# Kernel tuning notes

Hardware: AMD Instinct MI355X
Metric: run time of the kernel (lower is better)

The kernel has to match this reference:

```python
import jax, jax.numpy as jnp
import numpy as np
import math

B, S, D, H = 4, 1024, 1024, 16
HD = D // H  # head_size = 64
NEG = -1e9


def setup_inputs() -> dict:
    rng = jax.random.key(0)
    ks = jax.random.split(rng, 12)
    f = lambda k, shape: jax.random.normal(k, shape, dtype=jnp.float32)
    inp = {
        "query": f(ks[0], (B, S, D)),
        "key": f(ks[1], (B, S, D)),
        "value": f(ks[2], (B, S, D)),
        # rel: correlation matrix between interactions, non-negative
        "rel": jax.random.uniform(ks[3], (B, S, S), dtype=jnp.float32),
        "l1": jnp.float32(0.5),
        "l2": jnp.float32(0.5),
        # timestamp: |t_i - t_j| time gaps
        "timestamp": jax.random.uniform(ks[4], (B, S, S), dtype=jnp.float32) * 10.0,
        "encode_pos": 0,
        "pos_key_embeds": f(ks[5], (32, HD)) * 0.02,
        "pos_value_embeds": f(ks[6], (32, HD)) * 0.02,
        # causal mask: True = disallowed (future) position
        "mask": jnp.broadcast_to(jnp.triu(jnp.ones((S, S), dtype=bool), k=1), (B, S, S)),
        "Wq": f(ks[7], (D, D)) / math.sqrt(D), "bq": jnp.zeros((D,), jnp.float32),
        "Wk": f(ks[8], (D, D)) / math.sqrt(D), "bk": jnp.zeros((D,), jnp.float32),
        "Wv": f(ks[9], (D, D)) / math.sqrt(D), "bv": jnp.zeros((D,), jnp.float32),
    }
    return inp


def _split_heads(x, W, b):
    # nn.Linear uses x @ W.T + b ; reshape to [B,H,S,HD]
    y = x @ W.T + b
    return y.reshape(B, S, H, HD).transpose(0, 2, 1, 3)


def reference(query, key, value, rel, l1, l2, timestamp, encode_pos,
              pos_key_embeds, pos_value_embeds, mask,
              Wq, bq, Wk, bk, Wv, bv):
    assert encode_pos == 0, "reference implements the encode_pos=False path"
    q = _split_heads(query, Wq, bq)   # [B,H,S,HD]
    k = _split_heads(key, Wk, bk)
    v = _split_heads(value, Wv, bv)

    m = mask[:, None]  # [B,1,S,S], True = masked

    # relation-based attention: future-mask rel, softmax over nonzero entries
    relm = rel[:, None] * (~m).astype(jnp.float32)          # [B,1,S,S]
    rel_attn = jax.nn.softmax(jnp.where(relm == 0, -1e5, relm), axis=-1)

    # scaled dot-product scores
    scores = jnp.einsum("bhqd,bhkd->bhqk", q, k) / jnp.sqrt(jnp.float32(HD))
    scores = jnp.where(m, NEG, scores)
    prob_attn = jax.nn.softmax(scores, axis=-1)             # [B,H,S,S]

    # time-decay attention: exp(-|dt|), future-masked
    ts = jnp.exp(-jnp.abs(timestamp))[:, None]              # [B,1,S,S]
    ts = jnp.where(m, NEG, ts)
    time_attn = jax.nn.softmax(ts, axis=-1)

    prob = (1.0 - l2) * prob_attn + l2 * time_attn
    prob = (1.0 - l1) * prob + l1 * rel_attn                # [B,H,S,S]

    out = jnp.einsum("bhqk,bhkd->bhqd", prob, v)
    out = out.transpose(0, 2, 1, 3).reshape(B, S, D)
    return out, prob
```

## Files before the change

kernel.cpp:

```cpp
#include <hip/hip_runtime.h>
#include <cstdint>
#include <cstddef>


typedef __bf16 bf16_t;
typedef __bf16 bf16x8 __attribute__((ext_vector_type(8)));
typedef __bf16 bf16x4 __attribute__((ext_vector_type(4)));
typedef float  f32x4  __attribute__((ext_vector_type(4)));

__device__ __forceinline__ f32x4 mfma16(bf16x8 a, bf16x8 b, f32x4 c) {
  return __builtin_amdgcn_mfma_f32_16x16x32_bf16(a, b, c, 0, 0, 0);
}

__device__ __forceinline__ void g2l16(const void* g, void* l) {
  __builtin_amdgcn_global_load_lds((__attribute__((address_space(1))) void*)(g),
                                   (__attribute__((address_space(3))) void*)(l),
                                   16, 0, 0);
}

__global__ __launch_bounds__(256) void cast_kernel(
    const float* __restrict__ q, const float* __restrict__ k, const float* __restrict__ v,
    const float* __restrict__ wq, const float* __restrict__ wk, const float* __restrict__ wv,
    bf16_t* __restrict__ Xb, bf16_t* __restrict__ Wb) {
  int i = blockIdx.x * 256 + threadIdx.x;
  const float* src;
  bf16_t* dst;
  if (i < 3145728) {
    int m = i >> 20;
    size_t o = (size_t)(i & 1048575) * 4;
    src = (m == 0) ? q : (m == 1) ? k : v;
    dst = Xb + (size_t)m * 4194304 + o;
    src += o;
  } else {
    int j = i - 3145728;
    int m = j >> 18;
    size_t o = (size_t)(j & 262143) * 4;
    src = (m == 0) ? wq : (m == 1) ? wk : wv;
    dst = Wb + (size_t)m * 1048576 + o;
    src += o;
  }
  f32x4 f = *(const f32x4*)src;
  bf16x4 r;
  r[0] = (bf16_t)f[0]; r[1] = (bf16_t)f[1]; r[2] = (bf16_t)f[2]; r[3] = (bf16_t)f[3];
  *(bf16x4*)dst = r;
}

__global__ __launch_bounds__(256) void gemm_qkv(
    const bf16_t* __restrict__ Xb, const bf16_t* __restrict__ Wb,
    const float* __restrict__ bqp, const float* __restrict__ bkp, const float* __restrict__ bvp,
    bf16_t* __restrict__ Yb) {
  __shared__ __align__(16) bf16_t As[128 * 32];
  __shared__ __align__(16) bf16_t Bs[128 * 32];
  const int z = blockIdx.z;
  const bf16_t* X = Xb + (size_t)z * 4194304;
  const bf16_t* W = Wb + (size_t)z * 1048576;
  const float* bias = (z == 0) ? bqp : (z == 1) ? bkp : bvp;
  bf16_t* Y = Yb + (size_t)z * 4194304;

  const int tid = threadIdx.x;
  const int lane = tid & 63;
  const int w = tid >> 6;
  const int wr = w >> 1, wc = w & 1;
  const int rb = blockIdx.y * 128, cb = blockIdx.x * 128;
  const int lr = lane & 15, g = lane >> 4;

  f32x4 zero = {0.f, 0.f, 0.f, 0.f};
  f32x4 acc[4][4];
  for (int m = 0; m < 4; ++m)
    for (int n = 0; n < 4; ++n) acc[m][n] = zero;

  for (int k0 = 0; k0 < 1024; k0 += 32) {
    for (int r = 0; r < 2; ++r) {
      int cid = r * 256 + tid;
      int row = cid >> 2;
      int ko = (cid & 3) * 8;
      const bf16_t* ga = X + ((size_t)(rb + row) * 1024 + k0 + ko);
      const bf16_t* gb = W + ((size_t)(cb + row) * 1024 + k0 + ko);
      char* la = (char*)As + r * 4096 + w * 1024;
      char* lb = (char*)Bs + r * 4096 + w * 1024;
      g2l16(ga, la);
      g2l16(gb, lb);
    }
    asm volatile("s_waitcnt vmcnt(0)" ::: "memory");
    __syncthreads();

    bf16x8 afr[4], bfr[4];
    for (int m = 0; m < 4; ++m)
      afr[m] = *(const bf16x8*)&As[(wr * 64 + m * 16 + lr) * 32 + g * 8];
    for (int n = 0; n < 4; ++n)
      bfr[n] = *(const bf16x8*)&Bs[(wc * 64 + n * 16 + lr) * 32 + g * 8];
    for (int m = 0; m < 4; ++m)
      for (int n = 0; n < 4; ++n)
        acc[m][n] = mfma16(afr[m], bfr[n], acc[m][n]);
    __syncthreads();
  }

  for (int m = 0; m < 4; ++m) {
    int rowb = rb + wr * 64 + m * 16 + g * 4;
    for (int n = 0; n < 4; ++n) {
      int col = cb + wc * 64 + n * 16 + lr;
      float bb = bias[col];
      for (int r = 0; r < 4; ++r)
        Y[(size_t)(rowb + r) * 1024 + col] = (bf16_t)(acc[m][n][r] + bb);
    }
  }
}

__global__ __launch_bounds__(256) void transpose_v(const bf16_t* __restrict__ Yv,
                                                   bf16_t* __restrict__ vT) {
  __shared__ __align__(16) bf16_t t[64][68];
  const int bh = blockIdx.y, b = bh >> 4, h = bh & 15;
  const int s0 = blockIdx.x * 64;
  const int tid = threadIdx.x;
  for (int i = 0; i < 4; ++i) {
    int c = tid + i * 256;
    int r = c >> 4, c4 = (c & 15) * 4;
    bf16x4 v4 = *(const bf16x4*)(Yv + ((size_t)(b * 1024 + s0 + r)) * 1024 + h * 64 + c4);
    *(bf16x4*)&t[r][c4] = v4;
  }
  __syncthreads();
  for (int i = 0; i < 4; ++i) {
    int c = tid + i * 256;
    int hd = c >> 4, s4 = (c & 15) * 4;
    bf16x4 o;
    o[0] = t[s4 + 0][hd]; o[1] = t[s4 + 1][hd];
    o[2] = t[s4 + 2][hd]; o[3] = t[s4 + 3][hd];
    *(bf16x4*)(vT + ((size_t)(bh * 64 + hd)) * 1024 + s0 + s4) = o;
  }
}

__global__ __launch_bounds__(256) void base_kernel(
    const float* __restrict__ rel, const float* __restrict__ ts,
    const float* __restrict__ l1p, const float* __restrict__ l2p,
    bf16_t* __restrict__ baseb) {
  const int row = blockIdx.x;
  const int q = row & 1023;
  const int tid = threadIdx.x;
  const int w = tid >> 6;
  const float l1 = *l1p, l2 = *l2p;
  const float cr = l1, ct = (1.f - l1) * l2;

  f32x4 rv = *(const f32x4*)(rel + (size_t)row * 1024 + tid * 4);
  f32x4 tv = *(const f32x4*)(ts  + (size_t)row * 1024 + tid * 4);

  float x[4], t[4];
  for (int j = 0; j < 4; ++j) {
    int k = tid * 4 + j;
    bool msk = k > q;
    float rj = rv[j];
    x[j] = (msk || rj == 0.f) ? -100000.f : rj;
    t[j] = msk ? -1e9f : __expf(-fabsf(tv[j]));
  }
  float mr = fmaxf(fmaxf(x[0], x[1]), fmaxf(x[2], x[3]));
  float mt = fmaxf(fmaxf(t[0], t[1]), fmaxf(t[2], t[3]));
  for (int o = 1; o < 64; o <<= 1) {
    mr = fmaxf(mr, __shfl_xor(mr, o));
    mt = fmaxf(mt, __shfl_xor(mt, o));
  }
  __shared__ float red[4][4];
  if ((tid & 63) == 0) { red[0][w] = mr; red[1][w] = mt; }
  __syncthreads();
  mr = fmaxf(fmaxf(red[0][0], red[0][1]), fmaxf(red[0][2], red[0][3]));
  mt = fmaxf(fmaxf(red[1][0], red[1][1]), fmaxf(red[1][2], red[1][3]));

  float er[4], et[4], sr = 0.f, st = 0.f;
  for (int j = 0; j < 4; ++j) {
    er[j] = __expf(x[j] - mr);
    et[j] = __expf(t[j] - mt);
    sr += er[j]; st += et[j];
  }
  for (int o = 1; o < 64; o <<= 1) {
    sr += __shfl_xor(sr, o);
    st += __shfl_xor(st, o);
  }
  if ((tid & 63) == 0) { red[2][w] = sr; red[3][w] = st; }
  __syncthreads();
  sr = red[2][0] + red[2][1] + red[2][2] + red[2][3];
  st = red[3][0] + red[3][1] + red[3][2] + red[3][3];

  float isr = cr / sr, ist = ct / st;
  bf16x4 o4;
  for (int j = 0; j < 4; ++j) o4[j] = (bf16_t)(er[j] * isr + et[j] * ist);
  *(bf16x4*)(baseb + (size_t)row * 1024 + tid * 4) = o4;
}

__global__ __launch_bounds__(512) void attn_kernel(
    const bf16_t* __restrict__ qY, const bf16_t* __restrict__ kY,
    const bf16_t* __restrict__ vT, const bf16_t* __restrict__ baseb,
    const float* __restrict__ l1p, const float* __restrict__ l2p,
    float* __restrict__ outp, float* __restrict__ probp) {
  const int bid = blockIdx.x;
  const int j = bid >> 3;
  const int bh = (bid & 7) * 8 + (j & 7);
  const int qg = 31 - (j >> 3);
  const int b = bh >> 4, h = bh & 15;
  const int q0 = qg * 32;
  const int tid = threadIdx.x, lane = tid & 63, w = tid >> 6;
  const int t = w >> 2;
  const int cw = w & 3;
  const int lr = lane & 15, g = lane >> 4;
  const int qr = q0 + t * 16 + lr;
  const float l1 = *l1p, l2 = *l2p;
  const float c1 = (1.f - l1) * (1.f - l2);

  __shared__ __align__(16) union ShMem {
    bf16_t plds[8][16][36];
    float  pvred[8][16][64];
  } sh;
  __shared__ float zred[8][16];

  const bf16_t* qbase = qY + ((size_t)(b * 1024 + qr)) * 1024 + h * 64 + g * 8;
  bf16x8 bq0 = *(const bf16x8*)qbase;
  bf16x8 bq1 = *(const bf16x8*)(qbase + 32);

  const bf16_t* kptr = kY + ((size_t)(b * 1024 + lr)) * 1024 + h * 64 + g * 8;

  const int nch = (q0 + t * 16) / 32 + 1;
  f32x4 zero = {0.f, 0.f, 0.f, 0.f};

  bf16x4 esave[8][2];
  float zp = 0.f;
#pragma unroll
  for (int c = 0; c < 8; ++c) {
    const int ch = cw + 4 * c;
    if (ch < nch) {
      const bf16_t* p0 = kptr + (size_t)ch * 32768;
      bf16x8 k0 = *(const bf16x8*)p0;
      bf16x8 k1 = *(const bf16x8*)(p0 + 32);
      bf16x8 k2 = *(const bf16x8*)(p0 + 16384);
      bf16x8 k3 = *(const bf16x8*)(p0 + 16416);
      f32x4 s0 = zero, s1 = zero;
      s0 = mfma16(k0, bq0, s0);
      s0 = mfma16(k1, bq1, s0);
      s1 = mfma16(k2, bq0, s1);
      s1 = mfma16(k3, bq1, s1);
      const int kc0 = ch * 32 + g * 4;
      bf16x4 e0, e1;
      for (int r = 0; r < 4; ++r) {
        float ea = (kc0 + r > qr) ? 0.f : __expf(s0[r] * 0.125f);
        float eb = (kc0 + 16 + r > qr) ? 0.f : __expf(s1[r] * 0.125f);
        zp += ea + eb;
        e0[r] = (bf16_t)ea;
        e1[r] = (bf16_t)eb;
      }
      esave[c][0] = e0;
      esave[c][1] = e1;
    }
  }
  zp += __shfl_xor(zp, 16);
  zp += __shfl_xor(zp, 32);
  if (lane < 16) zred[w][lr] = zp;
  __syncthreads();
  const float Z = zred[t * 4 + 0][lr] + zred[t * 4 + 1][lr] +
                  zred[t * 4 + 2][lr] + zred[t * 4 + 3][lr];
  const float invz = c1 / Z;

  const bf16_t* baserow = baseb + ((size_t)(b * 1024 + qr)) * 1024;
  const bf16_t* vbase = vT + ((size_t)(bh * 64 + lr)) * 1024 + g * 8;
  float* probbase = probp + ((size_t)(bh * 1024 + q0 + t * 16)) * 1024;
  const int srow = lane >> 3, scol = (lane & 7) * 4;

  f32x4 acc[4];
  for (int cf = 0; cf < 4; ++cf) acc[cf] = zero;

#pragma unroll
  for (int c = 0; c < 8; ++c) {
    const int ch = cw + 4 * c;
    if (ch < nch) {
      bf16x8 vv[4];
      for (int cf = 0; cf < 4; ++cf)
        vv[cf] = *(const bf16x8*)(vbase + (size_t)cf * 16384 + ch * 32);
      for (int f = 0; f < 2; ++f) {
        const int kc0 = ch * 32 + f * 16 + g * 4;
        bf16x4 b4 = *(const bf16x4*)(baserow + kc0);
        bf16x4 eb = esave[c][f];
        bf16x4 pb;
        for (int r = 0; r < 4; ++r)
          pb[r] = (bf16_t)((float)eb[r] * invz + (float)b4[r]);
        *(bf16x4*)&sh.plds[w][lr][f * 16 + g * 4] = pb;
      }
      asm volatile("s_waitcnt lgkmcnt(0)" ::: "memory");
      bf16x8 pa = *(const bf16x8*)&sh.plds[w][lr][g * 8];
      bf16x4 r0 = *(const bf16x4*)&sh.plds[w][srow][scol];
      bf16x4 r1 = *(const bf16x4*)&sh.plds[w][srow + 8][scol];
      f32x4 o0, o1;
      for (int jj = 0; jj < 4; ++jj) { o0[jj] = (float)r0[jj]; o1[jj] = (float)r1[jj]; }
      float* pr = probbase + (size_t)srow * 1024 + ch * 32 + scol;
      __builtin_nontemporal_store(o0, (f32x4*)pr);
      __builtin_nontemporal_store(o1, (f32x4*)(pr + 8 * 1024));
      for (int cf = 0; cf < 4; ++cf)
        acc[cf] = mfma16(pa, vv[cf], acc[cf]);
    }
  }

  const int kstart = nch * 32;
  for (int i = 0; i < 4; ++i) {
    int qrr = q0 + t * 16 + cw * 4 + i;
    const bf16_t* brow = baseb + ((size_t)(b * 1024 + qrr)) * 1024;
    float* prow = probp + ((size_t)(bh * 1024 + qrr)) * 1024;
    for (int k = kstart + lane * 4; k < 1024; k += 256) {
      bf16x4 b4 = *(const bf16x4*)(brow + k);
      f32x4 f4;
      f4[0] = (float)b4[0]; f4[1] = (float)b4[1];
      f4[2] = (float)b4[2]; f4[3] = (float)b4[3];
      __builtin_nontemporal_store(f4, (f32x4*)(prow + k));
    }
  }

  __syncthreads();
  for (int cf = 0; cf < 4; ++cf)
    for (int r = 0; r < 4; ++r)
      sh.pvred[w][g * 4 + r][cf * 16 + lr] = acc[cf][r];
  __syncthreads();
  {
    const int gw = tid >> 6, hd = tid & 63;
    const int tt = gw >> 2;
    for (int i = 0; i < 4; ++i) {
      int rr = (gw & 3) * 4 + i;
      float s = sh.pvred[tt * 4 + 0][rr][hd] + sh.pvred[tt * 4 + 1][rr][hd] +
                sh.pvred[tt * 4 + 2][rr][hd] + sh.pvred[tt * 4 + 3][rr][hd];
      outp[((size_t)(b * 1024 + q0 + tt * 16 + rr)) * 1024 + h * 64 + hd] = s;
    }
  }
}

extern "C" void kernel_launch(void* const* d_in, const int* in_sizes, int n_in,
                              void* d_out, int out_size, void* d_ws, size_t ws_size,
                              hipStream_t stream) {
  const float* query = (const float*)d_in[0];
  const float* key   = (const float*)d_in[1];
  const float* value = (const float*)d_in[2];
  const float* rel   = (const float*)d_in[3];
  const float* l1p   = (const float*)d_in[4];
  const float* l2p   = (const float*)d_in[5];
  const float* tsp   = (const float*)d_in[6];
  const float* Wq = (const float*)d_in[11];
  const float* bq = (const float*)d_in[12];
  const float* Wk = (const float*)d_in[13];
  const float* bk = (const float*)d_in[14];
  const float* Wv = (const float*)d_in[15];
  const float* bv = (const float*)d_in[16];

  char* ws = (char*)d_ws;
  bf16_t* Xb    = (bf16_t*)(ws);
  bf16_t* Wb    = (bf16_t*)(ws + 25165824);
  bf16_t* Yb    = (bf16_t*)(ws + 31457280);
  bf16_t* vT    = (bf16_t*)(ws + 56623104);
  bf16_t* baseb = (bf16_t*)(ws + 65011712);

  float* outp  = (float*)d_out;
  float* probp = outp + 4194304;

  cast_kernel<<<dim3(15360), dim3(256), 0, stream>>>(query, key, value, Wq, Wk, Wv, Xb, Wb);
  gemm_qkv<<<dim3(8, 32, 3), dim3(256), 0, stream>>>(Xb, Wb, bq, bk, bv, Yb);
  transpose_v<<<dim3(16, 64), dim3(256), 0, stream>>>(Yb + (size_t)2 * 4194304, vT);
  base_kernel<<<dim3(4096), dim3(256), 0, stream>>>(rel, tsp, l1p, l2p, baseb);
  attn_kernel<<<dim3(2048), dim3(512), 0, stream>>>(Yb, Yb + 4194304, vT, baseb,
                                                    l1p, l2p, outp, probp);
}
```

Before: 171.9 us.

## Fuse fp32-to-bf16 cast into QKV GEMM and hoist attention loads out of branches

Removes the separate cast kernel: the QKV GEMM now reads fp32 inputs and weights directly, converts them in registers and stores bf16 into LDS, replacing the async global-to-LDS path. This saves one kernel launch and a full bf16 write and re-read of the activations and weights, at the cost of the GEMM loading twice the bytes per tile with synchronous register staging. In the attention kernel, the K, V and base loads are hoisted ahead of the causal branch using clamped chunk indices so they can be issued early. It also adds a launch-bounds occupancy hint, splits the Z accumulation across four lanes, and drops an explicit LDS waitcnt.

```diff
diff --git a/kernel.cpp b/kernel.cpp
--- a/kernel.cpp
+++ b/kernel.cpp
@@ -12,48 +12,16 @@
   return __builtin_amdgcn_mfma_f32_16x16x32_bf16(a, b, c, 0, 0, 0);
 }
 
-__device__ __forceinline__ void g2l16(const void* g, void* l) {
-  __builtin_amdgcn_global_load_lds((__attribute__((address_space(1))) void*)(g),
-                                   (__attribute__((address_space(3))) void*)(l),
-                                   16, 0, 0);
-}
-
-__global__ __launch_bounds__(256) void cast_kernel(
-    const float* __restrict__ q, const float* __restrict__ k, const float* __restrict__ v,
-    const float* __restrict__ wq, const float* __restrict__ wk, const float* __restrict__ wv,
-    bf16_t* __restrict__ Xb, bf16_t* __restrict__ Wb) {
-  int i = blockIdx.x * 256 + threadIdx.x;
-  const float* src;
-  bf16_t* dst;
-  if (i < 3145728) {
-    int m = i >> 20;
-    size_t o = (size_t)(i & 1048575) * 4;
-    src = (m == 0) ? q : (m == 1) ? k : v;
-    dst = Xb + (size_t)m * 4194304 + o;
-    src += o;
-  } else {
-    int j = i - 3145728;
-    int m = j >> 18;
-    size_t o = (size_t)(j & 262143) * 4;
-    src = (m == 0) ? wq : (m == 1) ? wk : wv;
-    dst = Wb + (size_t)m * 1048576 + o;
-    src += o;
-  }
-  f32x4 f = *(const f32x4*)src;
-  bf16x4 r;
-  r[0] = (bf16_t)f[0]; r[1] = (bf16_t)f[1]; r[2] = (bf16_t)f[2]; r[3] = (bf16_t)f[3];
-  *(bf16x4*)dst = r;
-}
-
 __global__ __launch_bounds__(256) void gemm_qkv(
-    const bf16_t* __restrict__ Xb, const bf16_t* __restrict__ Wb,
+    const float* __restrict__ qf, const float* __restrict__ kf, const float* __restrict__ vf,
+    const float* __restrict__ wqf, const float* __restrict__ wkf, const float* __restrict__ wvf,
     const float* __restrict__ bqp, const float* __restrict__ bkp, const float* __restrict__ bvp,
     bf16_t* __restrict__ Yb) {
   __shared__ __align__(16) bf16_t As[128 * 32];
   __shared__ __align__(16) bf16_t Bs[128 * 32];
   const int z = blockIdx.z;
-  const bf16_t* X = Xb + (size_t)z * 4194304;
-  const bf16_t* W = Wb + (size_t)z * 1048576;
+  const float* X = (z == 0) ? qf : (z == 1) ? kf : vf;
+  const float* W = (z == 0) ? wqf : (z == 1) ? wkf : wvf;
   const float* bias = (z == 0) ? bqp : (z == 1) ? bkp : bvp;
   bf16_t* Y = Yb + (size_t)z * 4194304;
 
@@ -74,14 +42,20 @@
       int cid = r * 256 + tid;
       int row = cid >> 2;
       int ko = (cid & 3) * 8;
-      const bf16_t* ga = X + ((size_t)(rb + row) * 1024 + k0 + ko);
-      const bf16_t* gb = W + ((size_t)(cb + row) * 1024 + k0 + ko);
-      char* la = (char*)As + r * 4096 + w * 1024;
-      char* lb = (char*)Bs + r * 4096 + w * 1024;
-      g2l16(ga, la);
-      g2l16(gb, lb);
-    }
-    asm volatile("s_waitcnt vmcnt(0)" ::: "memory");
+      const float* ga = X + ((size_t)(rb + row) * 1024 + k0 + ko);
+      const float* gb = W + ((size_t)(cb + row) * 1024 + k0 + ko);
+      f32x4 a0 = *(const f32x4*)ga;
+      f32x4 a1 = *(const f32x4*)(ga + 4);
+      f32x4 b0 = *(const f32x4*)gb;
+      f32x4 b1 = *(const f32x4*)(gb + 4);
+      bf16x8 av, bv8;
+      for (int j = 0; j < 4; ++j) {
+        av[j] = (bf16_t)a0[j]; av[4 + j] = (bf16_t)a1[j];
+        bv8[j] = (bf16_t)b0[j]; bv8[4 + j] = (bf16_t)b1[j];
+      }
+      *(bf16x8*)&As[row * 32 + ko] = av;
+      *(bf16x8*)&Bs[row * 32 + ko] = bv8;
+    }
     __syncthreads();
 
     bf16x8 afr[4], bfr[4];
@@ -184,7 +158,7 @@
   *(bf16x4*)(baseb + (size_t)row * 1024 + tid * 4) = o4;
 }
 
-__global__ __launch_bounds__(512) void attn_kernel(
+__global__ __launch_bounds__(512, 8) void attn_kernel(
     const bf16_t* __restrict__ qY, const bf16_t* __restrict__ kY,
     const bf16_t* __restrict__ vT, const bf16_t* __restrict__ baseb,
     const float* __restrict__ l1p, const float* __restrict__ l2p,
@@ -219,16 +193,17 @@
   f32x4 zero = {0.f, 0.f, 0.f, 0.f};
 
   bf16x4 esave[8][2];
-  float zp = 0.f;
+  f32x4 zacc = zero;
 #pragma unroll
   for (int c = 0; c < 8; ++c) {
     const int ch = cw + 4 * c;
+    const int cl = (ch < nch) ? ch : nch - 1;
+    const bf16_t* p0 = kptr + (size_t)cl * 32768;
+    bf16x8 k0 = *(const bf16x8*)p0;
+    bf16x8 k1 = *(const bf16x8*)(p0 + 32);
+    bf16x8 k2 = *(const bf16x8*)(p0 + 16384);
+    bf16x8 k3 = *(const bf16x8*)(p0 + 16416);
     if (ch < nch) {
-      const bf16_t* p0 = kptr + (size_t)ch * 32768;
-      bf16x8 k0 = *(const bf16x8*)p0;
-      bf16x8 k1 = *(const bf16x8*)(p0 + 32);
-      bf16x8 k2 = *(const bf16x8*)(p0 + 16384);
-      bf16x8 k3 = *(const bf16x8*)(p0 + 16416);
       f32x4 s0 = zero, s1 = zero;
       s0 = mfma16(k0, bq0, s0);
       s0 = mfma16(k1, bq1, s0);
@@ -239,7 +214,8 @@
       for (int r = 0; r < 4; ++r) {
         float ea = (kc0 + r > qr) ? 0.f : __expf(s0[r] * 0.125f);
         float eb = (kc0 + 16 + r > qr) ? 0.f : __expf(s1[r] * 0.125f);
-        zp += ea + eb;
+        zacc[r] += ea;
+        zacc[r] += eb;
         e0[r] = (bf16_t)ea;
         e1[r] = (bf16_t)eb;
       }
@@ -247,6 +223,7 @@
       esave[c][1] = e1;
     }
   }
+  float zp = (zacc[0] + zacc[1]) + (zacc[2] + zacc[3]);
   zp += __shfl_xor(zp, 16);
   zp += __shfl_xor(zp, 32);
   if (lane < 16) zred[w][lr] = zp;
@@ -266,20 +243,20 @@
 #pragma unroll
   for (int c = 0; c < 8; ++c) {
     const int ch = cw + 4 * c;
+    const int cl = (ch < nch) ? ch : nch - 1;
+    bf16x8 vv[4];
+    for (int cf = 0; cf < 4; ++cf)
+      vv[cf] = *(const bf16x8*)(vbase + (size_t)cf * 16384 + cl * 32);
+    bf16x4 b40 = *(const bf16x4*)(baserow + cl * 32 + g * 4);
+    bf16x4 b41 = *(const bf16x4*)(baserow + cl * 32 + 16 + g * 4);
     if (ch < nch) {
-      bf16x8 vv[4];
-      for (int cf = 0; cf < 4; ++cf)
-        vv[cf] = *(const bf16x8*)(vbase + (size_t)cf * 16384 + ch * 32);
-      for (int f = 0; f < 2; ++f) {
-        const int kc0 = ch * 32 + f * 16 + g * 4;
-        bf16x4 b4 = *(const bf16x4*)(baserow + kc0);
-        bf16x4 eb = esave[c][f];
-        bf16x4 pb;
-        for (int r = 0; r < 4; ++r)
-          pb[r] = (bf16_t)((float)eb[r] * invz + (float)b4[r]);
-        *(bf16x4*)&sh.plds[w][lr][f * 16 + g * 4] = pb;
+      bf16x4 pb0, pb1;
+      for (int r = 0; r < 4; ++r) {
+        pb0[r] = (bf16_t)((float)esave[c][0][r] * invz + (float)b40[r]);
+        pb1[r] = (bf16_t)((float)esave[c][1][r] * invz + (float)b41[r]);
       }
-      asm volatile("s_waitcnt lgkmcnt(0)" ::: "memory");
+      *(bf16x4*)&sh.plds[w][lr][g * 4] = pb0;
+      *(bf16x4*)&sh.plds[w][lr][16 + g * 4] = pb1;
       bf16x8 pa = *(const bf16x8*)&sh.plds[w][lr][g * 8];
       bf16x4 r0 = *(const bf16x4*)&sh.plds[w][srow][scol];
       bf16x4 r1 = *(const bf16x4*)&sh.plds[w][srow + 8][scol];
@@ -342,17 +319,15 @@
   const float* bv = (const float*)d_in[16];
 
   char* ws = (char*)d_ws;
-  bf16_t* Xb    = (bf16_t*)(ws);
-  bf16_t* Wb    = (bf16_t*)(ws + 25165824);
-  bf16_t* Yb    = (bf16_t*)(ws + 31457280);
-  bf16_t* vT    = (bf16_t*)(ws + 56623104);
-  bf16_t* baseb = (bf16_t*)(ws + 65011712);
+  bf16_t* Yb    = (bf16_t*)(ws);
+  bf16_t* vT    = (bf16_t*)(ws + 25165824);
+  bf16_t* baseb = (bf16_t*)(ws + 33554432);
 
   float* outp  = (float*)d_out;
   float* probp = outp + 4194304;
 
-  cast_kernel<<<dim3(15360), dim3(256), 0, stream>>>(query, key, value, Wq, Wk, Wv, Xb, Wb);
-  gemm_qkv<<<dim3(8, 32, 3), dim3(256), 0, stream>>>(Xb, Wb, bq, bk, bv, Yb);
+  gemm_qkv<<<dim3(8, 32, 3), dim3(256), 0, stream>>>(query, key, value, Wq, Wk, Wv,
+                                                     bq, bk, bv, Yb);
   transpose_v<<<dim3(16, 64), dim3(256), 0, stream>>>(Yb + (size_t)2 * 4194304, vT);
   base_kernel<<<dim3(4096), dim3(256), 0, stream>>>(rel, tsp, l1p, l2p, baseb);
   attn_kernel<<<dim3(2048), dim3(512), 0, stream>>>(Yb, Yb + 4194304, vT, baseb,
```

Result: slower. 193.9 us (+12.8%).

## Fuse V transpose into QKV GEMM epilogue and double GEMM K-step

Applied to the files above, without the earlier changes.

The separate transpose_v kernel is removed. The QKV GEMM epilogue for the V projection now writes each 4-row accumulator fragment straight into the head-major transposed vT layout, which saves a kernel launch and a round trip of V through global memory. The GEMM main loop also loads a 64-wide K slab per barrier pair instead of 32, which halves the number of synchronisations but doubles the shared memory per block and may lower occupancy.

```diff
diff --git a/kernel.cpp b/kernel.cpp
--- a/kernel.cpp
+++ b/kernel.cpp
@@ -48,9 +48,9 @@
 __global__ __launch_bounds__(256) void gemm_qkv(
     const bf16_t* __restrict__ Xb, const bf16_t* __restrict__ Wb,
     const float* __restrict__ bqp, const float* __restrict__ bkp, const float* __restrict__ bvp,
-    bf16_t* __restrict__ Yb) {
-  __shared__ __align__(16) bf16_t As[128 * 32];
-  __shared__ __align__(16) bf16_t Bs[128 * 32];
+    bf16_t* __restrict__ Yb, bf16_t* __restrict__ vT) {
+  __shared__ __align__(16) bf16_t As[2 * 128 * 32];
+  __shared__ __align__(16) bf16_t Bs[2 * 128 * 32];
   const int z = blockIdx.z;
   const bf16_t* X = Xb + (size_t)z * 4194304;
   const bf16_t* W = Wb + (size_t)z * 1048576;
@@ -69,63 +69,58 @@
   for (int m = 0; m < 4; ++m)
     for (int n = 0; n < 4; ++n) acc[m][n] = zero;
 
-  for (int k0 = 0; k0 < 1024; k0 += 32) {
-    for (int r = 0; r < 2; ++r) {
-      int cid = r * 256 + tid;
-      int row = cid >> 2;
-      int ko = (cid & 3) * 8;
+  for (int k0 = 0; k0 < 1024; k0 += 64) {
+    for (int r = 0; r < 4; ++r) {
+      const int hh = r >> 1;
+      const int cid = (r & 1) * 256 + tid;
+      const int row = cid >> 2;
+      const int ko = (cid & 3) * 8 + hh * 32;
       const bf16_t* ga = X + ((size_t)(rb + row) * 1024 + k0 + ko);
       const bf16_t* gb = W + ((size_t)(cb + row) * 1024 + k0 + ko);
-      char* la = (char*)As + r * 4096 + w * 1024;
-      char* lb = (char*)Bs + r * 4096 + w * 1024;
+      char* la = (char*)As + hh * 8192 + (r & 1) * 4096 + w * 1024;
+      char* lb = (char*)Bs + hh * 8192 + (r & 1) * 4096 + w * 1024;
       g2l16(ga, la);
       g2l16(gb, lb);
     }
     asm volatile("s_waitcnt vmcnt(0)" ::: "memory");
     __syncthreads();
 
-    bf16x8 afr[4], bfr[4];
-    for (int m = 0; m < 4; ++m)
-      afr[m] = *(const bf16x8*)&As[(wr * 64 + m * 16 + lr) * 32 + g * 8];
-    for (int n = 0; n < 4; ++n)
-      bfr[n] = *(const bf16x8*)&Bs[(wc * 64 + n * 16 + lr) * 32 + g * 8];
-    for (int m = 0; m < 4; ++m)
+    for (int kk = 0; kk < 2; ++kk) {
+      bf16x8 afr[4], bfr[4];
+      for (int m = 0; m < 4; ++m)
+        afr[m] = *(const bf16x8*)&As[kk * 4096 + (wr * 64 + m * 16 + lr) * 32 + g * 8];
       for (int n = 0; n < 4; ++n)
-        acc[m][n] = mfma16(afr[m], bfr[n], acc[m][n]);
+        bfr[n] = *(const bf16x8*)&Bs[kk * 4096 + (wc * 64 + n * 16 + lr) * 32 + g * 8];
+      for (int m = 0; m < 4; ++m)
+        for (int n = 0; n < 4; ++n)
+          acc[m][n] = mfma16(afr[m], bfr[n], acc[m][n]);
+    }
     __syncthreads();
   }
 
-  for (int m = 0; m < 4; ++m) {
-    int rowb = rb + wr * 64 + m * 16 + g * 4;
-    for (int n = 0; n < 4; ++n) {
-      int col = cb + wc * 64 + n * 16 + lr;
-      float bb = bias[col];
-      for (int r = 0; r < 4; ++r)
-        Y[(size_t)(rowb + r) * 1024 + col] = (bf16_t)(acc[m][n][r] + bb);
-    }
-  }
-}
-
-__global__ __launch_bounds__(256) void transpose_v(const bf16_t* __restrict__ Yv,
-                                                   bf16_t* __restrict__ vT) {
-  __shared__ __align__(16) bf16_t t[64][68];
-  const int bh = blockIdx.y, b = bh >> 4, h = bh & 15;
-  const int s0 = blockIdx.x * 64;
-  const int tid = threadIdx.x;
-  for (int i = 0; i < 4; ++i) {
-    int c = tid + i * 256;
-    int r = c >> 4, c4 = (c & 15) * 4;
-    bf16x4 v4 = *(const bf16x4*)(Yv + ((size_t)(b * 1024 + s0 + r)) * 1024 + h * 64 + c4);
-    *(bf16x4*)&t[r][c4] = v4;
-  }
-  __syncthreads();
-  for (int i = 0; i < 4; ++i) {
-    int c = tid + i * 256;
-    int hd = c >> 4, s4 = (c & 15) * 4;
-    bf16x4 o;
-    o[0] = t[s4 + 0][hd]; o[1] = t[s4 + 1][hd];
-    o[2] = t[s4 + 2][hd]; o[3] = t[s4 + 3][hd];
-    *(bf16x4*)(vT + ((size_t)(bh * 64 + hd)) * 1024 + s0 + s4) = o;
+  if (z == 2) {
+    for (int m = 0; m < 4; ++m) {
+      const int rowb = rb + wr * 64 + m * 16 + g * 4;
+      const int bb = rowb >> 10;
+      const int s0 = rowb & 1023;
+      for (int n = 0; n < 4; ++n) {
+        const int col = cb + wc * 64 + n * 16 + lr;
+        const float bv = bias[col];
+        bf16x4 o;
+        for (int r = 0; r < 4; ++r) o[r] = (bf16_t)(acc[m][n][r] + bv);
+        *(bf16x4*)(vT + ((size_t)((bb * 16 + (col >> 6)) * 64 + (col & 63))) * 1024 + s0) = o;
+      }
+    }
+  } else {
+    for (int m = 0; m < 4; ++m) {
+      const int rowb = rb + wr * 64 + m * 16 + g * 4;
+      for (int n = 0; n < 4; ++n) {
+        const int col = cb + wc * 64 + n * 16 + lr;
+        const float bv = bias[col];
+        for (int r = 0; r < 4; ++r)
+          Y[(size_t)(rowb + r) * 1024 + col] = (bf16_t)(acc[m][n][r] + bv);
+      }
+    }
   }
 }
 
@@ -352,8 +347,7 @@
   float* probp = outp + 4194304;
 
   cast_kernel<<<dim3(15360), dim3(256), 0, stream>>>(query, key, value, Wq, Wk, Wv, Xb, Wb);
-  gemm_qkv<<<dim3(8, 32, 3), dim3(256), 0, stream>>>(Xb, Wb, bq, bk, bv, Yb);
-  transpose_v<<<dim3(16, 64), dim3(256), 0, stream>>>(Yb + (size_t)2 * 4194304, vT);
+  gemm_qkv<<<dim3(8, 32, 3), dim3(256), 0, stream>>>(Xb, Wb, bq, bk, bv, Yb, vT);
   base_kernel<<<dim3(4096), dim3(256), 0, stream>>>(rel, tsp, l1p, l2p, baseb);
   attn_kernel<<<dim3(2048), dim3(512), 0, stream>>>(Yb, Yb + 4194304, vT, baseb,
                                                     l1p, l2p, outp, probp);
```

Measured after the change: 179.4 us. 1.04x slower.

## Split PV into unnormalized-exp and base terms computed in the score pass

Applied to the files above, without the earlier changes.

The P·V product is split into two accumulators. One holds the unnormalized exp scores times V, the other holds the precomputed base-probability term times V, and both are built in the first pass over key chunks. The softmax normalization is applied per row at the final reduction, so the second pass only writes prob rows directly from registers and no longer reloads V or goes through the LDS transpose. In exchange it doubles the MFMA work for PV, keeps more registers live, and writes prob with narrower per-lane 16-byte segments instead of the previously transposed, more coalesced layout.

```diff
diff --git a/kernel.cpp b/kernel.cpp
--- a/kernel.cpp
+++ b/kernel.cpp
@@ -214,11 +214,15 @@
   bf16x8 bq1 = *(const bf16x8*)(qbase + 32);
 
   const bf16_t* kptr = kY + ((size_t)(b * 1024 + lr)) * 1024 + h * 64 + g * 8;
+  const bf16_t* baserow = baseb + ((size_t)(b * 1024 + qr)) * 1024;
+  const bf16_t* vbase = vT + ((size_t)(bh * 64 + lr)) * 1024 + g * 8;
 
   const int nch = (q0 + t * 16) / 32 + 1;
   f32x4 zero = {0.f, 0.f, 0.f, 0.f};
 
   bf16x4 esave[8][2];
+  f32x4 accE[4], accB[4];
+  for (int cf = 0; cf < 4; ++cf) { accE[cf] = zero; accB[cf] = zero; }
   float zp = 0.f;
 #pragma unroll
   for (int c = 0; c < 8; ++c) {
@@ -229,11 +233,17 @@
       bf16x8 k1 = *(const bf16x8*)(p0 + 32);
       bf16x8 k2 = *(const bf16x8*)(p0 + 16384);
       bf16x8 k3 = *(const bf16x8*)(p0 + 16416);
+      bf16x8 vv[4];
+      for (int cf = 0; cf < 4; ++cf)
+        vv[cf] = *(const bf16x8*)(vbase + (size_t)cf * 16384 + ch * 32);
+      bf16x8 bfr = *(const bf16x8*)(baserow + ch * 32 + g * 8);
       f32x4 s0 = zero, s1 = zero;
       s0 = mfma16(k0, bq0, s0);
       s0 = mfma16(k1, bq1, s0);
       s1 = mfma16(k2, bq0, s1);
       s1 = mfma16(k3, bq1, s1);
+      for (int cf = 0; cf < 4; ++cf)
+        accB[cf] = mfma16(bfr, vv[cf], accB[cf]);
       const int kc0 = ch * 32 + g * 4;
       bf16x4 e0, e1;
       for (int r = 0; r < 4; ++r) {
@@ -245,6 +255,12 @@
       }
       esave[c][0] = e0;
       esave[c][1] = e1;
+      *(bf16x4*)&sh.plds[w][lr][g * 4] = e0;
+      *(bf16x4*)&sh.plds[w][lr][16 + g * 4] = e1;
+      asm volatile("s_waitcnt lgkmcnt(0)" ::: "memory");
+      bf16x8 pa = *(const bf16x8*)&sh.plds[w][lr][g * 8];
+      for (int cf = 0; cf < 4; ++cf)
+        accE[cf] = mfma16(pa, vv[cf], accE[cf]);
     }
   }
   zp += __shfl_xor(zp, 16);
@@ -255,41 +271,20 @@
                   zred[t * 4 + 2][lr] + zred[t * 4 + 3][lr];
   const float invz = c1 / Z;
 
-  const bf16_t* baserow = baseb + ((size_t)(b * 1024 + qr)) * 1024;
-  const bf16_t* vbase = vT + ((size_t)(bh * 64 + lr)) * 1024 + g * 8;
-  float* probbase = probp + ((size_t)(bh * 1024 + q0 + t * 16)) * 1024;
-  const int srow = lane >> 3, scol = (lane & 7) * 4;
-
-  f32x4 acc[4];
-  for (int cf = 0; cf < 4; ++cf) acc[cf] = zero;
-
+  float* probrow = probp + ((size_t)(bh * 1024 + qr)) * 1024;
 #pragma unroll
   for (int c = 0; c < 8; ++c) {
     const int ch = cw + 4 * c;
     if (ch < nch) {
-      bf16x8 vv[4];
-      for (int cf = 0; cf < 4; ++cf)
-        vv[cf] = *(const bf16x8*)(vbase + (size_t)cf * 16384 + ch * 32);
       for (int f = 0; f < 2; ++f) {
         const int kc0 = ch * 32 + f * 16 + g * 4;
         bf16x4 b4 = *(const bf16x4*)(baserow + kc0);
         bf16x4 eb = esave[c][f];
-        bf16x4 pb;
+        f32x4 p;
         for (int r = 0; r < 4; ++r)
-          pb[r] = (bf16_t)((float)eb[r] * invz + (float)b4[r]);
-        *(bf16x4*)&sh.plds[w][lr][f * 16 + g * 4] = pb;
+          p[r] = (float)eb[r] * invz + (float)b4[r];
+        __builtin_nontemporal_store(p, (f32x4*)(probrow + kc0));
       }
-      asm volatile("s_waitcnt lgkmcnt(0)" ::: "memory");
-      bf16x8 pa = *(const bf16x8*)&sh.plds[w][lr][g * 8];
-      bf16x4 r0 = *(const bf16x4*)&sh.plds[w][srow][scol];
-      bf16x4 r1 = *(const bf16x4*)&sh.plds[w][srow + 8][scol];
-      f32x4 o0, o1;
-      for (int jj = 0; jj < 4; ++jj) { o0[jj] = (float)r0[jj]; o1[jj] = (float)r1[jj]; }
-      float* pr = probbase + (size_t)srow * 1024 + ch * 32 + scol;
-      __builtin_nontemporal_store(o0, (f32x4*)pr);
-      __builtin_nontemporal_store(o1, (f32x4*)(pr + 8 * 1024));
-      for (int cf = 0; cf < 4; ++cf)
-        acc[cf] = mfma16(pa, vv[cf], acc[cf]);
     }
   }
 
@@ -308,9 +303,14 @@
   }
 
   __syncthreads();
-  for (int cf = 0; cf < 4; ++cf)
-    for (int r = 0; r < 4; ++r)
-      sh.pvred[w][g * 4 + r][cf * 16 + lr] = acc[cf][r];
+  for (int r = 0; r < 4; ++r) {
+    const int row = g * 4 + r;
+    const float Zr = zred[t * 4 + 0][row] + zred[t * 4 + 1][row] +
+                     zred[t * 4 + 2][row] + zred[t * 4 + 3][row];
+    const float ivr = c1 / Zr;
+    for (int cf = 0; cf < 4; ++cf)
+      sh.pvred[w][row][cf * 16 + lr] = accE[cf][r] * ivr + accB[cf][r];
+  }
   __syncthreads();
   {
     const int gw = tid >> 6, hd = tid & 63;
```

New measurement: 211.7 us. 1.23x slower.
